# Kernel optimization log

Hardware: AMD Instinct MI355X
Metric: run time of the kernel (lower is better)

Reference implementation:

```python
import jax, jax.numpy as jnp
import numpy as np
from jax import lax

D_MODEL = 768; DEPTH = 12; HEADS = 12; HEAD_D = 64; PATCH = 16; IMG = 224
NTOK = (IMG // PATCH) ** 2 + 1  # 197
BATCH = 32; K_PATCHES = 5; EPS = 1e-6


def setup_inputs() -> dict:
    key = jax.random.key(0)
    ks = jax.random.split(key, 16)
    rn = lambda i, shape, s=1.0: jax.random.normal(ks[i], shape, jnp.float32) * s
    return {
        'x': rn(0, (BATCH, 3, IMG, IMG)),
        'patch_w': rn(1, (D_MODEL, 3, PATCH, PATCH), 0.02),
        'patch_b': jnp.zeros((D_MODEL,), jnp.float32),
        'cls_token': rn(2, (1, 1, D_MODEL), 0.02),
        'pos_embed': rn(3, (1, NTOK, D_MODEL), 0.02),
        'ln1_w': jnp.ones((DEPTH, D_MODEL), jnp.float32),
        'ln1_b': jnp.zeros((DEPTH, D_MODEL), jnp.float32),
        'qkv_w': rn(4, (DEPTH, 3 * D_MODEL, D_MODEL), 0.02),
        'qkv_b': jnp.zeros((DEPTH, 3 * D_MODEL), jnp.float32),
        'proj_w': rn(5, (DEPTH, D_MODEL, D_MODEL), 0.02),
        'proj_b': jnp.zeros((DEPTH, D_MODEL), jnp.float32),
        'pk_param': rn(6, (DEPTH, HEADS, HEAD_D), 0.02),
        'pv_param': rn(7, (DEPTH, HEADS, HEAD_D), 0.02),
        'prompt_k': rn(8, (DEPTH, HEADS, HEAD_D), 0.02),
        'prompt_v': rn(9, (DEPTH, HEADS, HEAD_D), 0.02),
        'ln2_w': jnp.ones((DEPTH, D_MODEL), jnp.float32),
        'ln2_b': jnp.zeros((DEPTH, D_MODEL), jnp.float32),
        'fc1_w': rn(10, (DEPTH, 4 * D_MODEL, D_MODEL), 0.02),
        'fc1_b': jnp.zeros((DEPTH, 4 * D_MODEL), jnp.float32),
        'fc2_w': rn(11, (DEPTH, D_MODEL, 4 * D_MODEL), 0.02),
        'fc2_b': jnp.zeros((DEPTH, D_MODEL), jnp.float32),
        'norm_w': jnp.ones((D_MODEL,), jnp.float32),
        'norm_b': jnp.zeros((D_MODEL,), jnp.float32),
        'k_patches': K_PATCHES,
    }


def _layer_norm(h, w, b):
    mu = h.mean(-1, keepdims=True)
    var = ((h - mu) ** 2).mean(-1, keepdims=True)
    return (h - mu) * lax.rsqrt(var + EPS) * w + b


def reference(x, patch_w, patch_b, cls_token, pos_embed, ln1_w, ln1_b, qkv_w, qkv_b,
              proj_w, proj_b, pk_param, pv_param, prompt_k, prompt_v, ln2_w, ln2_b,
              fc1_w, fc1_b, fc2_w, fc2_b, norm_w, norm_b, k_patches):
    B = x.shape[0]
    C, H, D = D_MODEL, HEADS, HEAD_D
    scale = D ** -0.5
    # patch embedding: conv stride=patch -> [B, C, 14, 14] -> [B, 196, C]
    p = lax.conv_general_dilated(x, patch_w, (PATCH, PATCH), 'VALID',
                                 dimension_numbers=('NCHW', 'OIHW', 'NCHW'))
    p = p.reshape(B, C, -1).transpose(0, 2, 1) + patch_b
    tokens = jnp.concatenate([jnp.broadcast_to(cls_token, (B, 1, C)), p], axis=1) + pos_embed
    N = tokens.shape[1]
    batch_idx = jnp.arange(B)[:, None]

    for l in range(DEPTH):
        h = _layer_norm(tokens, ln1_w[l], ln1_b[l])
        qkv = (h @ qkv_w[l].T + qkv_b[l]).reshape(B, N, 3, H, D).transpose(2, 0, 3, 1, 4)
        q, k, v = qkv[0], qkv[1], qkv[2]  # [B,H,N,D]
        # probe attention: softmax is row-wise, only the CLS row is used downstream
        probe = jax.nn.softmax(jnp.einsum('bhd,bhkd->bhk', q[:, :, 0], k) * scale, axis=-1)
        cls_scores = probe.mean(axis=1)[:, 1:]  # [B, N-1]
        topk_idx = lax.top_k(cls_scores, k_patches)[1] + 1  # [B, k] in [1, N)
        sel = jnp.zeros((B, N), tokens.dtype).at[batch_idx, topk_idx].add(1.0)  # [B,N]
        # prompt override of CLS k/v + scatter-add of learned patch prompts at top-k patches
        k_mod = k.at[:, :, 0, :].add(prompt_k[l]) + sel[:, None, :, None] * pk_param[l][None, :, None, :]
        v_mod = v.at[:, :, 0, :].add(prompt_v[l]) + sel[:, None, :, None] * pv_param[l][None, :, None, :]
        attn = jax.nn.softmax(jnp.einsum('bhqd,bhkd->bhqk', q, k_mod) * scale, axis=-1)
        out = jnp.einsum('bhqk,bhkd->bhqd', attn, v_mod).transpose(0, 2, 1, 3).reshape(B, N, C)
        tokens = tokens + (out @ proj_w[l].T + proj_b[l])
        h2 = _layer_norm(tokens, ln2_w[l], ln2_b[l])
        m = jax.nn.gelu(h2 @ fc1_w[l].T + fc1_b[l], approximate=False) @ fc2_w[l].T + fc2_b[l]
        tokens = tokens + m

    return _layer_norm(tokens, norm_w, norm_b)
```

## Files before the change

### kernel.cpp

```cpp
#include <hip/hip_runtime.h>
#include <math.h>

#define DMODEL 768
#define DEPTH 12
#define HEADS 12
#define HEADD 64
#define NTOK 197
#define BATCH 32
#define NPATCH 196
#define MTOK (BATCH * NTOK)
#define MPAT (BATCH * NPATCH)
#define QKVD 2304
#define MLPD 3072

typedef unsigned short u16;
typedef __attribute__((ext_vector_type(8))) short bf16x8;
typedef __attribute__((ext_vector_type(4))) float f32x4;

#define OFF_QKV 0
#define OFF_PROJ (QKVD * DMODEL)
#define OFF_FC1 (OFF_PROJ + DMODEL * DMODEL)
#define OFF_FC2 (OFF_FC1 + MLPD * DMODEL)
#define WTOTAL (OFF_FC2 + DMODEL * MLPD)

__device__ __forceinline__ u16 bf16r(float x) {
  union { float f; unsigned u; } c; c.f = x;
  unsigned u = c.u + 0x7FFF + ((c.u >> 16) & 1);
  return (u16)(u >> 16);
}
__device__ __forceinline__ float gelu_f(float x) {
  return 0.5f * x * (1.f + erff(x * 0.70710678118654752440f));
}
__device__ __forceinline__ void gload16(const void* g, void* l) {
  __builtin_amdgcn_global_load_lds(
      (const __attribute__((address_space(1))) void*)g,
      (__attribute__((address_space(3))) void*)l, 16, 0, 0);
}

__device__ __forceinline__ float blk_red_sum(float v, float* red) {
#pragma unroll
  for (int o = 32; o; o >>= 1) v += __shfl_xor(v, o);
  __syncthreads();
  if ((threadIdx.x & 63) == 0) red[threadIdx.x >> 6] = v;
  __syncthreads();
  return red[0] + red[1] + red[2] + red[3];
}
__device__ __forceinline__ float blk_red_max(float v, float* red) {
#pragma unroll
  for (int o = 32; o; o >>= 1) v = fmaxf(v, __shfl_xor(v, o));
  __syncthreads();
  if ((threadIdx.x & 63) == 0) red[threadIdx.x >> 6] = v;
  __syncthreads();
  return fmaxf(fmaxf(red[0], red[1]), fmaxf(red[2], red[3]));
}

__global__ __launch_bounds__(256) void convert_bf16(const float* __restrict__ in,
                                                    u16* __restrict__ out, int n) {
  int i = (blockIdx.x * 256 + threadIdx.x) * 4;
  if (i >= n) return;
  float4 v = *(const float4*)(in + i);
  ushort4 o;
  o.x = bf16r(v.x); o.y = bf16r(v.y); o.z = bf16r(v.z); o.w = bf16r(v.w);
  *(ushort4*)(out + i) = o;
}

__global__ __launch_bounds__(256) void convert_layer_w(
    const float* __restrict__ qkv_w, const float* __restrict__ proj_w,
    const float* __restrict__ fc1_w, const float* __restrict__ fc2_w,
    u16* __restrict__ wbuf) {
  int i = (blockIdx.x * 256 + threadIdx.x) * 4;
  if (i >= WTOTAL) return;
  const float* s;
  if (i < OFF_PROJ) s = qkv_w + i;
  else if (i < OFF_FC1) s = proj_w + (i - OFF_PROJ);
  else if (i < OFF_FC2) s = fc1_w + (i - OFF_FC1);
  else s = fc2_w + (i - OFF_FC2);
  float4 v = *(const float4*)s;
  ushort4 o;
  o.x = bf16r(v.x); o.y = bf16r(v.y); o.z = bf16r(v.z); o.w = bf16r(v.w);
  *(ushort4*)(wbuf + i) = o;
}

__global__ __launch_bounds__(256) void im2col(const float* __restrict__ x,
                                              u16* __restrict__ col) {
  int idx = blockIdx.x * 256 + threadIdx.x;
  if (idx >= MPAT * DMODEL) return;
  int kk = idx % DMODEL;
  int m = idx / DMODEL;
  int bb = m / NPATCH, p = m % NPATCH;
  int ph = p / 14, pw = p % 14;
  int ch = kk >> 8, rem = kk & 255;
  int i = rem >> 4, j = rem & 15;
  col[idx] = bf16r(x[(((size_t)bb * 3 + ch) * 224 + ph * 16 + i) * 224 + pw * 16 + j]);
}

__global__ __launch_bounds__(256) void assemble(const float* __restrict__ pat,
                                                const float* __restrict__ cls,
                                                const float* __restrict__ pos,
                                                float* __restrict__ tokens) {
  int idx = blockIdx.x * 256 + threadIdx.x;
  if (idx >= MTOK * DMODEL) return;
  int c = idx % DMODEL;
  int t = idx / DMODEL;
  int bb = t / NTOK, n = t % NTOK;
  float v;
  if (n == 0) v = cls[c];
  else v = pat[((size_t)bb * NPATCH + (n - 1)) * DMODEL + c];
  tokens[idx] = v + pos[n * DMODEL + c];
}

template <bool BF16OUT>
__global__ __launch_bounds__(256) void layernorm(const float* __restrict__ in,
                                                 const float* __restrict__ w,
                                                 const float* __restrict__ b,
                                                 void* __restrict__ outp) {
  __shared__ float red[4];
  const int t = blockIdx.x, tid = threadIdx.x;
  const float* r = in + (size_t)t * DMODEL;
  float x0 = r[tid], x1 = r[tid + 256], x2 = r[tid + 512];
  float mu = blk_red_sum(x0 + x1 + x2, red) * (1.f / 768.f);
  float d0 = x0 - mu, d1 = x1 - mu, d2 = x2 - mu;
  float var = blk_red_sum(d0 * d0 + d1 * d1 + d2 * d2, red) * (1.f / 768.f);
  float is = rsqrtf(var + 1e-6f);
  float v0 = d0 * is * w[tid] + b[tid];
  float v1 = d1 * is * w[tid + 256] + b[tid + 256];
  float v2 = d2 * is * w[tid + 512] + b[tid + 512];
  if (BF16OUT) {
    u16* o = (u16*)outp + (size_t)t * DMODEL;
    o[tid] = bf16r(v0); o[tid + 256] = bf16r(v1); o[tid + 512] = bf16r(v2);
  } else {
    float* o = (float*)outp + (size_t)t * DMODEL;
    o[tid] = v0; o[tid + 256] = v1; o[tid + 512] = v2;
  }
}

template <int MODE, int TN>
__global__ __launch_bounds__(256) void gemm3(const u16* __restrict__ A,
                                             const u16* __restrict__ B,
                                             const float* __restrict__ bias,
                                             void* __restrict__ C,
                                             int M, int N, int K) {
  constexpr int NJ = TN / 32;
  constexpr int LPT = (TN == 128) ? 4 : 3;
  __shared__ u16 As[3][128 * 32];
  __shared__ u16 Bs[3][TN * 32];
  const int tid = threadIdx.x;
  const int w = tid >> 6, lane = tid & 63;

  const int nwg = gridDim.x * gridDim.y;
  int lin = blockIdx.y * gridDim.x + blockIdx.x;
  {
    int q = nwg >> 3, r = nwg & 7;
    int xcd = lin & 7, idx = lin >> 3;
    lin = (xcd < r ? xcd * (q + 1) : r * (q + 1) + (xcd - r) * q) + idx;
  }
  const int ntn = gridDim.y;
  const int m0 = (lin / ntn) * 128, n0 = (lin % ntn) * TN;

  const int wr = (w >> 1) * 64, wc = (w & 1) * (TN / 2);
  f32x4 acc[4][NJ] = {};

  const int srow = tid >> 2;
  const int scol = ((tid & 3) ^ ((srow >> 1) & 3)) * 8;
  int ar0 = m0 + srow;       if (ar0 >= M) ar0 = M - 1;
  int ar1 = m0 + 64 + srow;  if (ar1 >= M) ar1 = M - 1;
  const u16* Ag0 = A + (size_t)ar0 * K + scol;
  const u16* Ag1 = A + (size_t)ar1 * K + scol;
  const u16* Bg0 = B + (size_t)(n0 + srow) * K + scol;
  const u16* Bg1 = B + (size_t)(n0 + (TN == 128 ? 64 : 0) + srow) * K + scol;

  auto STAGE = [&](int buf, int kk) {
    gload16(Ag0 + kk, &As[buf][w * 512]);
    gload16(Ag1 + kk, &As[buf][2048 + w * 512]);
    gload16(Bg0 + kk, &Bs[buf][w * 512]);
    if (TN == 128) gload16(Bg1 + kk, &Bs[buf][2048 + w * 512]);
  };

  const int fr = lane & 15, lq = lane >> 4;
  const int kq = (lq ^ ((fr >> 1) & 3)) * 8;

  const int nt = K >> 5;
  STAGE(0, 0);
  STAGE(1, 32);
  asm volatile("s_waitcnt vmcnt(%0)" ::"n"(LPT) : "memory");
  __builtin_amdgcn_s_barrier();
  __builtin_amdgcn_sched_barrier(0);

  for (int t = 0; t < nt; ++t) {
    const int cur = t % 3;
    bf16x8 af[4], bfr[NJ];
#pragma unroll
    for (int i = 0; i < 4; ++i)
      af[i] = *(const bf16x8*)&As[cur][(wr + i * 16 + fr) * 32 + kq];
#pragma unroll
    for (int j = 0; j < NJ; ++j)
      bfr[j] = *(const bf16x8*)&Bs[cur][(wc + j * 16 + fr) * 32 + kq];
    const bool more = (t + 2 < nt);
    if (more) STAGE((t + 2) % 3, (t + 2) * 32);
#pragma unroll
    for (int i = 0; i < 4; ++i)
#pragma unroll
      for (int j = 0; j < NJ; ++j)
        acc[i][j] = __builtin_amdgcn_mfma_f32_16x16x32_bf16(af[i], bfr[j],
                                                            acc[i][j], 0, 0, 0);
    if (more)
      asm volatile("s_waitcnt vmcnt(%0)" ::"n"(LPT) : "memory");
    else
      asm volatile("s_waitcnt vmcnt(0)" ::: "memory");
    __builtin_amdgcn_s_barrier();
    __builtin_amdgcn_sched_barrier(0);
  }

  const int fq = lq * 4;
#pragma unroll
  for (int j = 0; j < NJ; ++j) {
    const int n = n0 + wc + j * 16 + fr;
    const float bb = bias[n];
#pragma unroll
    for (int i = 0; i < 4; ++i) {
      const int mbase = m0 + wr + i * 16 + fq;
#pragma unroll
      for (int r = 0; r < 4; ++r) {
        const int m = mbase + r;
        if (m < M) {
          const float v = acc[i][j][r] + bb;
          if (MODE == 0) ((float*)C)[(size_t)m * N + n] = v;
          else if (MODE == 1) ((float*)C)[(size_t)m * N + n] += v;
          else ((u16*)C)[(size_t)m * N + n] = bf16r(gelu_f(v));
        }
      }
    }
  }
}

__global__ __launch_bounds__(256) void probe_scores(const float* __restrict__ qkv,
                                                    float* __restrict__ probs) {
  __shared__ float qrow[64];
  __shared__ float s[NTOK];
  __shared__ float red[4];
  const int bh = blockIdx.x;
  const int b = bh / HEADS, h = bh % HEADS;
  const int tid = threadIdx.x;
  const size_t row0 = (size_t)b * NTOK * QKVD;
  if (tid < 64) qrow[tid] = qkv[row0 + h * HEADD + tid];
  __syncthreads();
  const int sub = tid & 3;
  for (int k = tid >> 2; k < NTOK; k += 64) {
    const float* kr = qkv + row0 + (size_t)k * QKVD + DMODEL + h * HEADD + sub * 16;
    float dot = 0.f;
#pragma unroll
    for (int c = 0; c < 4; ++c) {
      float4 kv = *(const float4*)(kr + c * 4);
      dot = fmaf(qrow[sub * 16 + c * 4 + 0], kv.x, dot);
      dot = fmaf(qrow[sub * 16 + c * 4 + 1], kv.y, dot);
      dot = fmaf(qrow[sub * 16 + c * 4 + 2], kv.z, dot);
      dot = fmaf(qrow[sub * 16 + c * 4 + 3], kv.w, dot);
    }
    dot += __shfl_xor(dot, 1);
    dot += __shfl_xor(dot, 2);
    if (sub == 0) s[k] = dot * 0.125f;
  }
  __syncthreads();
  float mx = -1e30f;
  for (int k = tid; k < NTOK; k += 256) mx = fmaxf(mx, s[k]);
  mx = blk_red_max(mx, red);
  float sm = 0.f;
  for (int k = tid; k < NTOK; k += 256) sm += expf(s[k] - mx);
  sm = blk_red_sum(sm, red);
  float inv = 1.f / sm;
  for (int k = tid; k < NTOK; k += 256)
    probs[(size_t)bh * NTOK + k] = expf(s[k] - mx) * inv;
}

__global__ __launch_bounds__(256) void topk_sel(const float* __restrict__ probs,
                                                const int* __restrict__ kpptr,
                                                int* __restrict__ topk) {
  __shared__ float accsc[NTOK];
  const int b = blockIdx.x, tid = threadIdx.x;
  for (int k = tid; k < NTOK; k += 256) {
    float a = 0.f;
#pragma unroll
    for (int h = 0; h < HEADS; ++h) a += probs[(size_t)(b * HEADS + h) * NTOK + k];
    accsc[k] = a;
  }
  __syncthreads();
  if (tid == 0) {
    int kpn = kpptr[0];
    if (kpn < 0) kpn = 0;
    if (kpn > 8) kpn = 8;
    for (int j = 0; j < kpn; ++j) {
      float best = -1e30f;
      int bi = 1;
      for (int k = 1; k < NTOK; ++k)
        if (accsc[k] > best) { best = accsc[k]; bi = k; }
      topk[b * 8 + j] = bi;
      accsc[bi] = -2e30f;
    }
    for (int j = kpn; j < 8; ++j) topk[b * 8 + j] = -1;
  }
}

__device__ __forceinline__ bf16x8 pack8(float4 a, float4 b) {
  bf16x8 r;
  r[0] = (short)bf16r(a.x); r[1] = (short)bf16r(a.y);
  r[2] = (short)bf16r(a.z); r[3] = (short)bf16r(a.w);
  r[4] = (short)bf16r(b.x); r[5] = (short)bf16r(b.y);
  r[6] = (short)bf16r(b.z); r[7] = (short)bf16r(b.w);
  return r;
}

__global__ __launch_bounds__(512, 1) void attn_mfma(
    const float* __restrict__ qkv, const float* __restrict__ prompt_k,
    const float* __restrict__ prompt_v, const float* __restrict__ pk,
    const float* __restrict__ pv, const int* __restrict__ topk,
    const int* __restrict__ kpptr, u16* __restrict__ outp) {
  __shared__ u16 Ks[208 * 64];
  __shared__ u16 Vs[64 * 256];
  __shared__ u16 Ps[8][16 * 256];
  __shared__ float selb[NTOK];
  const int bh = blockIdx.x;
  const int b = bh / HEADS, h = bh % HEADS;
  const int tid = threadIdx.x, w = tid >> 6, lane = tid & 63;
  const int fr = lane & 15, lq = lane >> 4;

  int kpn = kpptr[0];
  if (kpn < 0) kpn = 0;
  if (kpn > 8) kpn = 8;
  for (int k = tid; k < NTOK; k += 512) {
    float sl = 0.f;
    for (int j = 0; j < kpn; ++j)
      if (topk[b * 8 + j] == k) sl = 1.f;
    selb[k] = sl;
  }
  __syncthreads();

  const size_t row0 = (size_t)b * NTOK * QKVD;
  const float* kg = qkv + row0 + DMODEL + h * HEADD;
  const float* vg = qkv + row0 + 2 * DMODEL + h * HEADD;
  for (int idx = tid; idx < 208 * 64; idx += 512) {
    int tok = idx >> 6, d = idx & 63;
    float v = 0.f;
    if (tok < NTOK) {
      v = kg[(size_t)tok * QKVD + d] + selb[tok] * pk[h * HEADD + d];
      if (tok == 0) v += prompt_k[h * HEADD + d];
    }
    int off = (tok * 128 + d * 2) ^ ((tok & 7) << 4);
    *(u16*)((char*)Ks + off) = bf16r(v);
  }
  for (int idx = tid; idx < 224 * 64; idx += 512) {
    int tok = idx >> 6, d = idx & 63;
    float v = 0.f;
    if (tok < NTOK) {
      v = vg[(size_t)tok * QKVD + d] + selb[tok] * pv[h * HEADD + d];
      if (tok == 0) v += prompt_v[h * HEADD + d];
    }
    int off = (d * 512 + tok * 2) ^ ((d & 7) << 4);
    *(u16*)((char*)Vs + off) = bf16r(v);
  }
  __syncthreads();

  u16* Pw = Ps[w];
  u16* ob = outp + (size_t)b * NTOK * DMODEL + h * HEADD;

#pragma unroll
  for (int pass = 0; pass < 2; ++pass) {
    const int qt = pass * 8 + w;
    const bool active = (qt < 14);
    if (active) {
      int qrow = qt * 16 + fr;
      if (qrow > NTOK - 1) qrow = NTOK - 1;
      const float* qp = qkv + row0 + (size_t)qrow * QKVD + h * HEADD + lq * 8;
      bf16x8 aq0 = pack8(*(const float4*)qp, *(const float4*)(qp + 4));
      bf16x8 aq1 = pack8(*(const float4*)(qp + 32), *(const float4*)(qp + 36));
      f32x4 sa[13];
#pragma unroll
      for (int j = 0; j < 13; ++j) {
        int tok = j * 16 + fr;
        int o0 = (tok * 128 + lq * 16) ^ ((tok & 7) << 4);
        int o1 = (tok * 128 + 64 + lq * 16) ^ ((tok & 7) << 4);
        bf16x8 bk0 = *(const bf16x8*)((const char*)Ks + o0);
        bf16x8 bk1 = *(const bf16x8*)((const char*)Ks + o1);
        f32x4 z = {0.f, 0.f, 0.f, 0.f};
        z = __builtin_amdgcn_mfma_f32_16x16x32_bf16(aq0, bk0, z, 0, 0, 0);
        sa[j] = __builtin_amdgcn_mfma_f32_16x16x32_bf16(aq1, bk1, z, 0, 0, 0);
      }
      const bool v12 = (fr < 5);
      float m4[4] = {-1e30f, -1e30f, -1e30f, -1e30f};
#pragma unroll
      for (int j = 0; j < 13; ++j) {
        if (j == 12 && !v12) continue;
#pragma unroll
        for (int r = 0; r < 4; ++r) m4[r] = fmaxf(m4[r], sa[j][r] * 0.125f);
      }
#pragma unroll
      for (int o = 8; o; o >>= 1)
#pragma unroll
        for (int r = 0; r < 4; ++r) m4[r] = fmaxf(m4[r], __shfl_xor(m4[r], o));
      float s4[4] = {0.f, 0.f, 0.f, 0.f};
#pragma unroll
      for (int j = 0; j < 13; ++j) {
        const bool valid = (j < 12) || v12;
#pragma unroll
        for (int r = 0; r < 4; ++r) {
          float p = valid ? __expf(sa[j][r] * 0.125f - m4[r]) : 0.f;
          sa[j][r] = p;
          s4[r] += p;
        }
      }
#pragma unroll
      for (int o = 8; o; o >>= 1)
#pragma unroll
        for (int r = 0; r < 4; ++r) s4[r] += __shfl_xor(s4[r], o);
      float inv[4];
#pragma unroll
      for (int r = 0; r < 4; ++r) inv[r] = 1.f / s4[r];
#pragma unroll
      for (int r = 0; r < 4; ++r) {
        int row = lq * 4 + r;
        int rbase = row * 512, sw = (row & 7) << 4;
#pragma unroll
        for (int j = 0; j < 13; ++j) {
          int off = (rbase + (j * 16 + fr) * 2) ^ sw;
          *(u16*)((char*)Pw + off) = bf16r(sa[j][r] * inv[r]);
        }
        int offz = (rbase + (208 + fr) * 2) ^ sw;
        *(u16*)((char*)Pw + offz) = 0;
      }
    }
    __syncthreads();
    if (active) {
      f32x4 oa[4] = {};
#pragma unroll
      for (int kc = 0; kc < 7; ++kc) {
        int po = (fr * 512 + (kc * 32 + lq * 8) * 2) ^ ((fr & 7) << 4);
        bf16x8 pa = *(const bf16x8*)((const char*)Pw + po);
#pragma unroll
        for (int dt = 0; dt < 4; ++dt) {
          int d = dt * 16 + fr;
          int vo = (d * 512 + (kc * 32 + lq * 8) * 2) ^ ((d & 7) << 4);
          bf16x8 vb = *(const bf16x8*)((const char*)Vs + vo);
          oa[dt] = __builtin_amdgcn_mfma_f32_16x16x32_bf16(pa, vb, oa[dt], 0, 0, 0);
        }
      }
#pragma unroll
      for (int r = 0; r < 4; ++r) {
        int q = qt * 16 + lq * 4 + r;
        if (q < NTOK) {
          u16* orow = ob + (size_t)q * DMODEL;
#pragma unroll
          for (int dt = 0; dt < 4; ++dt) orow[dt * 16 + fr] = bf16r(oa[dt][r]);
        }
      }
    }
    __syncthreads();
  }
}

extern "C" void kernel_launch(void* const* d_in, const int* in_sizes, int n_in,
                              void* d_out, int out_size, void* d_ws, size_t ws_size,
                              hipStream_t stream) {
  const float* x = (const float*)d_in[0];
  const float* patch_w = (const float*)d_in[1];
  const float* patch_b = (const float*)d_in[2];
  const float* cls_tok = (const float*)d_in[3];
  const float* pos_emb = (const float*)d_in[4];
  const float* ln1_w = (const float*)d_in[5];
  const float* ln1_b = (const float*)d_in[6];
  const float* qkv_w = (const float*)d_in[7];
  const float* qkv_b = (const float*)d_in[8];
  const float* proj_w = (const float*)d_in[9];
  const float* proj_b = (const float*)d_in[10];
  const float* pk_par = (const float*)d_in[11];
  const float* pv_par = (const float*)d_in[12];
  const float* pr_k = (const float*)d_in[13];
  const float* pr_v = (const float*)d_in[14];
  const float* ln2_w = (const float*)d_in[15];
  const float* ln2_b = (const float*)d_in[16];
  const float* fc1_w = (const float*)d_in[17];
  const float* fc1_b = (const float*)d_in[18];
  const float* fc2_w = (const float*)d_in[19];
  const float* fc2_b = (const float*)d_in[20];
  const float* norm_w = (const float*)d_in[21];
  const float* norm_b = (const float*)d_in[22];
  const int* kp = (const int*)d_in[23];

  float* tokens = (float*)d_ws;
  float* bufh = tokens + (size_t)MTOK * DMODEL;
  float* bufbig = bufh + (size_t)MTOK * DMODEL;
  u16* wbuf = (u16*)(bufbig + (size_t)MTOK * MLPD);
  u16* im2colb = wbuf + WTOTAL;
  int* topk = (int*)(im2colb + (size_t)MPAT * DMODEL);
  float* probs = (float*)(topk + BATCH * 8);

  const int mt = (MTOK + 127) / 128;
  const int mtp = (MPAT + 127) / 128;

  convert_bf16<<<(DMODEL * DMODEL / 4 + 255) / 256, 256, 0, stream>>>(
      patch_w, wbuf, DMODEL * DMODEL);
  im2col<<<(MPAT * DMODEL + 255) / 256, 256, 0, stream>>>(x, im2colb);
  gemm3<0, 64><<<dim3(mtp, DMODEL / 64), 256, 0, stream>>>(
      im2colb, wbuf, patch_b, bufh, MPAT, DMODEL, DMODEL);
  assemble<<<(MTOK * DMODEL + 255) / 256, 256, 0, stream>>>(bufh, cls_tok,
                                                            pos_emb, tokens);

  for (int l = 0; l < DEPTH; ++l) {
    convert_layer_w<<<(WTOTAL / 4 + 255) / 256, 256, 0, stream>>>(
        qkv_w + (size_t)l * QKVD * DMODEL, proj_w + (size_t)l * DMODEL * DMODEL,
        fc1_w + (size_t)l * MLPD * DMODEL, fc2_w + (size_t)l * DMODEL * MLPD,
        wbuf);
    layernorm<true><<<MTOK, 256, 0, stream>>>(tokens, ln1_w + l * DMODEL,
                                              ln1_b + l * DMODEL, bufh);
    gemm3<0, 128><<<dim3(mt, QKVD / 128), 256, 0, stream>>>(
        (const u16*)bufh, wbuf + OFF_QKV, qkv_b + l * QKVD, bufbig,
        MTOK, QKVD, DMODEL);
    probe_scores<<<BATCH * HEADS, 256, 0, stream>>>(bufbig, probs);
    topk_sel<<<BATCH, 256, 0, stream>>>(probs, kp, topk);
    attn_mfma<<<BATCH * HEADS, 512, 0, stream>>>(
        bufbig, pr_k + l * HEADS * HEADD, pr_v + l * HEADS * HEADD,
        pk_par + l * HEADS * HEADD, pv_par + l * HEADS * HEADD, topk, kp,
        (u16*)bufh);
    gemm3<1, 64><<<dim3(mt, DMODEL / 64), 256, 0, stream>>>(
        (const u16*)bufh, wbuf + OFF_PROJ, proj_b + l * DMODEL, tokens,
        MTOK, DMODEL, DMODEL);
    layernorm<true><<<MTOK, 256, 0, stream>>>(tokens, ln2_w + l * DMODEL,
                                              ln2_b + l * DMODEL, bufh);
    gemm3<2, 128><<<dim3(mt, MLPD / 128), 256, 0, stream>>>(
        (const u16*)bufh, wbuf + OFF_FC1, fc1_b + l * MLPD, bufbig,
        MTOK, MLPD, DMODEL);
    gemm3<1, 64><<<dim3(mt, DMODEL / 64), 256, 0, stream>>>(
        (const u16*)bufbig, wbuf + OFF_FC2, fc2_b + l * DMODEL, tokens,
        MTOK, DMODEL, MLPD);
  }
  layernorm<false><<<MTOK, 256, 0, stream>>>(tokens, norm_w, norm_b, d_out);
}
```

Before: 3.863 ms.

## Batch weight conversion, use wave-per-row layernorm, and reorder GEMM prefetch

Converts all layers' weights to bf16 in a single launch when the workspace is large enough, replacing twelve per-layer conversion launches. Rewrites layernorm so that one 64-lane wave handles one row, using vectorized float4 loads and shuffle reductions in place of shared-memory block reductions. In the GEMM, the global prefetch of the next stage is issued before the LDS fragment reads, and the sched_barriers are removed so the compiler can interleave instructions. The single-launch conversion depends on workspace size and falls back to the per-layer path otherwise; the workspace layout uses hardcoded byte offsets.

After: 4.072 ms. 1.05x slower.

```diff
diff --git a/kernel.cpp b/kernel.cpp
--- a/kernel.cpp
+++ b/kernel.cpp
@@ -81,6 +81,24 @@
   *(ushort4*)(wbuf + i) = o;
 }
 
+__global__ __launch_bounds__(256) void convert_all_w(
+    const float* __restrict__ qkv_w, const float* __restrict__ proj_w,
+    const float* __restrict__ fc1_w, const float* __restrict__ fc2_w,
+    u16* __restrict__ wall) {
+  const int l = blockIdx.y;
+  int i = (blockIdx.x * 256 + threadIdx.x) * 4;
+  if (i >= WTOTAL) return;
+  const float* s;
+  if (i < OFF_PROJ) s = qkv_w + (size_t)l * QKVD * DMODEL + i;
+  else if (i < OFF_FC1) s = proj_w + (size_t)l * DMODEL * DMODEL + (i - OFF_PROJ);
+  else if (i < OFF_FC2) s = fc1_w + (size_t)l * MLPD * DMODEL + (i - OFF_FC1);
+  else s = fc2_w + (size_t)l * DMODEL * MLPD + (i - OFF_FC2);
+  float4 v = *(const float4*)s;
+  ushort4 o;
+  o.x = bf16r(v.x); o.y = bf16r(v.y); o.z = bf16r(v.z); o.w = bf16r(v.w);
+  *(ushort4*)(wall + (size_t)l * WTOTAL + i) = o;
+}
+
 __global__ __launch_bounds__(256) void im2col(const float* __restrict__ x,
                                               u16* __restrict__ col) {
   int idx = blockIdx.x * 256 + threadIdx.x;
@@ -110,27 +128,54 @@
 }
 
 template <bool BF16OUT>
-__global__ __launch_bounds__(256) void layernorm(const float* __restrict__ in,
-                                                 const float* __restrict__ w,
-                                                 const float* __restrict__ b,
-                                                 void* __restrict__ outp) {
-  __shared__ float red[4];
-  const int t = blockIdx.x, tid = threadIdx.x;
-  const float* r = in + (size_t)t * DMODEL;
-  float x0 = r[tid], x1 = r[tid + 256], x2 = r[tid + 512];
-  float mu = blk_red_sum(x0 + x1 + x2, red) * (1.f / 768.f);
-  float d0 = x0 - mu, d1 = x1 - mu, d2 = x2 - mu;
-  float var = blk_red_sum(d0 * d0 + d1 * d1 + d2 * d2, red) * (1.f / 768.f);
-  float is = rsqrtf(var + 1e-6f);
-  float v0 = d0 * is * w[tid] + b[tid];
-  float v1 = d1 * is * w[tid + 256] + b[tid + 256];
-  float v2 = d2 * is * w[tid + 512] + b[tid + 512];
+__global__ __launch_bounds__(256) void layernorm_w(const float* __restrict__ in,
+                                                   const float* __restrict__ w,
+                                                   const float* __restrict__ b,
+                                                   void* __restrict__ outp,
+                                                   int ntok) {
+  const int wv = threadIdx.x >> 6, lane = threadIdx.x & 63;
+  const int t = blockIdx.x * 4 + wv;
+  if (t >= ntok) return;
+  const f32x4* r = (const f32x4*)(in + (size_t)t * DMODEL);
+  f32x4 x0 = r[lane], x1 = r[lane + 64], x2 = r[lane + 128];
+  float s = (x0[0] + x0[1] + x0[2] + x0[3]) + (x1[0] + x1[1] + x1[2] + x1[3]) +
+            (x2[0] + x2[1] + x2[2] + x2[3]);
+#pragma unroll
+  for (int o = 32; o; o >>= 1) s += __shfl_xor(s, o);
+  const float mu = s * (1.f / 768.f);
+  float vs = 0.f;
+#pragma unroll
+  for (int e = 0; e < 4; ++e) {
+    float d0 = x0[e] - mu, d1 = x1[e] - mu, d2 = x2[e] - mu;
+    vs += d0 * d0 + d1 * d1 + d2 * d2;
+  }
+#pragma unroll
+  for (int o = 32; o; o >>= 1) vs += __shfl_xor(vs, o);
+  const float is = rsqrtf(vs * (1.f / 768.f) + 1e-6f);
+  const f32x4* wp = (const f32x4*)w;
+  const f32x4* bp = (const f32x4*)b;
+  f32x4 w0 = wp[lane], w1 = wp[lane + 64], w2 = wp[lane + 128];
+  f32x4 b0 = bp[lane], b1 = bp[lane + 64], b2 = bp[lane + 128];
+  f32x4 y0, y1, y2;
+#pragma unroll
+  for (int e = 0; e < 4; ++e) {
+    y0[e] = (x0[e] - mu) * is * w0[e] + b0[e];
+    y1[e] = (x1[e] - mu) * is * w1[e] + b1[e];
+    y2[e] = (x2[e] - mu) * is * w2[e] + b2[e];
+  }
   if (BF16OUT) {
-    u16* o = (u16*)outp + (size_t)t * DMODEL;
-    o[tid] = bf16r(v0); o[tid + 256] = bf16r(v1); o[tid + 512] = bf16r(v2);
+    ushort4* o = (ushort4*)((u16*)outp + (size_t)t * DMODEL);
+    ushort4 q0, q1, q2;
+#pragma unroll
+    for (int e = 0; e < 4; ++e) {
+      ((u16*)&q0)[e] = bf16r(y0[e]);
+      ((u16*)&q1)[e] = bf16r(y1[e]);
+      ((u16*)&q2)[e] = bf16r(y2[e]);
+    }
+    o[lane] = q0; o[lane + 64] = q1; o[lane + 128] = q2;
   } else {
-    float* o = (float*)outp + (size_t)t * DMODEL;
-    o[tid] = v0; o[tid + 256] = v1; o[tid + 512] = v2;
+    f32x4* o = (f32x4*)((float*)outp + (size_t)t * DMODEL);
+    o[lane] = y0; o[lane + 64] = y1; o[lane + 128] = y2;
   }
 }
 
@@ -184,10 +229,11 @@
   STAGE(1, 32);
   asm volatile("s_waitcnt vmcnt(%0)" ::"n"(LPT) : "memory");
   __builtin_amdgcn_s_barrier();
-  __builtin_amdgcn_sched_barrier(0);
 
   for (int t = 0; t < nt; ++t) {
     const int cur = t % 3;
+    const bool more = (t + 2 < nt);
+    if (more) STAGE((t + 2) % 3, (t + 2) * 32);
     bf16x8 af[4], bfr[NJ];
 #pragma unroll
     for (int i = 0; i < 4; ++i)
@@ -195,8 +241,6 @@
 #pragma unroll
     for (int j = 0; j < NJ; ++j)
       bfr[j] = *(const bf16x8*)&Bs[cur][(wc + j * 16 + fr) * 32 + kq];
-    const bool more = (t + 2 < nt);
-    if (more) STAGE((t + 2) % 3, (t + 2) * 32);
 #pragma unroll
     for (int i = 0; i < 4; ++i)
 #pragma unroll
@@ -208,7 +252,6 @@
     else
       asm volatile("s_waitcnt vmcnt(0)" ::: "memory");
     __builtin_amdgcn_s_barrier();
-    __builtin_amdgcn_sched_barrier(0);
   }
 
   const int fq = lq * 4;
@@ -484,34 +527,46 @@
   const float* norm_b = (const float*)d_in[22];
   const int* kp = (const int*)d_in[23];
 
-  float* tokens = (float*)d_ws;
-  float* bufh = tokens + (size_t)MTOK * DMODEL;
-  float* bufbig = bufh + (size_t)MTOK * DMODEL;
-  u16* wbuf = (u16*)(bufbig + (size_t)MTOK * MLPD);
-  u16* im2colb = wbuf + WTOTAL;
-  int* topk = (int*)(im2colb + (size_t)MPAT * DMODEL);
-  float* probs = (float*)(topk + BATCH * 8);
+  char* base = (char*)d_ws;
+  float* tokens = (float*)base;
+  float* bufh = (float*)(base + 19365888ull);
+  float* bufbig = (float*)(base + 38731776ull);
+  u16* im2colb = (u16*)(base + 116195328ull);
+  u16* patchwb = (u16*)(base + 125829120ull);
+  int* topk = (int*)(base + 127008768ull);
+  float* probs = (float*)(base + 127009792ull);
+  u16* wbuf = (u16*)(base + 127312384ull);
+  const size_t WBYTES = (size_t)WTOTAL * 2;
+  const bool batch = ws_size >= 127312384ull + WBYTES * DEPTH;
 
   const int mt = (MTOK + 127) / 128;
   const int mtp = (MPAT + 127) / 128;
+  const int lnb = (MTOK + 3) / 4;
+
+  if (batch)
+    convert_all_w<<<dim3(WTOTAL / 1024, DEPTH), 256, 0, stream>>>(
+        qkv_w, proj_w, fc1_w, fc2_w, wbuf);
 
   convert_bf16<<<(DMODEL * DMODEL / 4 + 255) / 256, 256, 0, stream>>>(
-      patch_w, wbuf, DMODEL * DMODEL);
+      patch_w, patchwb, DMODEL * DMODEL);
   im2col<<<(MPAT * DMODEL + 255) / 256, 256, 0, stream>>>(x, im2colb);
   gemm3<0, 64><<<dim3(mtp, DMODEL / 64), 256, 0, stream>>>(
-      im2colb, wbuf, patch_b, bufh, MPAT, DMODEL, DMODEL);
+      im2colb, patchwb, patch_b, bufh, MPAT, DMODEL, DMODEL);
   assemble<<<(MTOK * DMODEL + 255) / 256, 256, 0, stream>>>(bufh, cls_tok,
                                                             pos_emb, tokens);
 
   for (int l = 0; l < DEPTH; ++l) {
-    convert_layer_w<<<(WTOTAL / 4 + 255) / 256, 256, 0, stream>>>(
-        qkv_w + (size_t)l * QKVD * DMODEL, proj_w + (size_t)l * DMODEL * DMODEL,
-        fc1_w + (size_t)l * MLPD * DMODEL, fc2_w + (size_t)l * DMODEL * MLPD,
-        wbuf);
-    layernorm<true><<<MTOK, 256, 0, stream>>>(tokens, ln1_w + l * DMODEL,
-                                              ln1_b + l * DMODEL, bufh);
+    u16* wl = batch ? (wbuf + (size_t)l * WTOTAL) : wbuf;
+    if (!batch)
+      convert_layer_w<<<(WTOTAL / 4 + 255) / 256, 256, 0, stream>>>(
+          qkv_w + (size_t)l * QKVD * DMODEL,
+          proj_w + (size_t)l * DMODEL * DMODEL,
+          fc1_w + (size_t)l * MLPD * DMODEL,
+          fc2_w + (size_t)l * DMODEL * MLPD, wl);
+    layernorm_w<true><<<lnb, 256, 0, stream>>>(tokens, ln1_w + l * DMODEL,
+                                               ln1_b + l * DMODEL, bufh, MTOK);
     gemm3<0, 128><<<dim3(mt, QKVD / 128), 256, 0, stream>>>(
-        (const u16*)bufh, wbuf + OFF_QKV, qkv_b + l * QKVD, bufbig,
+        (const u16*)bufh, wl + OFF_QKV, qkv_b + l * QKVD, bufbig,
         MTOK, QKVD, DMODEL);
     probe_scores<<<BATCH * HEADS, 256, 0, stream>>>(bufbig, probs);
     topk_sel<<<BATCH, 256, 0, stream>>>(probs, kp, topk);
@@ -520,16 +575,17 @@
         pk_par + l * HEADS * HEADD, pv_par + l * HEADS * HEADD, topk, kp,
         (u16*)bufh);
     gemm3<1, 64><<<dim3(mt, DMODEL / 64), 256, 0, stream>>>(
-        (const u16*)bufh, wbuf + OFF_PROJ, proj_b + l * DMODEL, tokens,
+        (const u16*)bufh, wl + OFF_PROJ, proj_b + l * DMODEL, tokens,
         MTOK, DMODEL, DMODEL);
-    layernorm<true><<<MTOK, 256, 0, stream>>>(tokens, ln2_w + l * DMODEL,
-                                              ln2_b + l * DMODEL, bufh);
+    layernorm_w<true><<<lnb, 256, 0, stream>>>(tokens, ln2_w + l * DMODEL,
+                                               ln2_b + l * DMODEL, bufh, MTOK);
     gemm3<2, 128><<<dim3(mt, MLPD / 128), 256, 0, stream>>>(
-        (const u16*)bufh, wbuf + OFF_FC1, fc1_b + l * MLPD, bufbig,
+        (const u16*)bufh, wl + OFF_FC1, fc1_b + l * MLPD, bufbig,
         MTOK, MLPD, DMODEL);
     gemm3<1, 64><<<dim3(mt, DMODEL / 64), 256, 0, stream>>>(
-        (const u16*)bufbig, wbuf + OFF_FC2, fc2_b + l * DMODEL, tokens,
+        (const u16*)bufbig, wl + OFF_FC2, fc2_b + l * DMODEL, tokens,
         MTOK, DMODEL, MLPD);
   }
-  layernorm<false><<<MTOK, 256, 0, stream>>>(tokens, norm_w, norm_b, d_out);
-}
+  layernorm_w<false><<<lnb, 256, 0, stream>>>(tokens, norm_w, norm_b, d_out,
+                                              MTOK);
+}
```
